# Kernel tuning notes

Hardware: AMD Instinct MI355X
Metric: run time of the kernel (lower is better)

## Reference

```python
import jax, jax.numpy as jnp
import numpy as np

B = 1_048_576
W = 64  # hidden width
N_FREQ = 6   # 3 dims * 6 freqs * (sin,cos) = 36
K_BLOB = 4   # one-blob bins per dim


def _freq_embed(p):
    # [B,3] -> [B,36]
    freqs = 2.0 ** jnp.arange(N_FREQ, dtype=p.dtype)
    ang = jnp.pi * p[:, :, None] * freqs  # [B,3,6]
    return jnp.concatenate([jnp.sin(ang), jnp.cos(ang)], axis=-1).reshape(p.shape[0], 3 * 2 * N_FREQ)


def _sph(d):
    # unit-square parameterization of a direction, [B,3] -> [B,2]
    d = d / (jnp.linalg.norm(d, axis=-1, keepdims=True) + 1e-8)
    u = jnp.arctan2(d[:, 1], d[:, 0]) / (2.0 * jnp.pi) + 0.5
    v = jnp.arccos(jnp.clip(d[:, 2], -1.0 + 1e-6, 1.0 - 1e-6)) / jnp.pi
    return jnp.stack([u, v], axis=-1)


def _one_blob(x, k=K_BLOB):
    # x in [0,1], [B,D] -> [B,D*k] Gaussian one-blob encoding
    centers = (jnp.arange(k, dtype=x.dtype) + 0.5) / k
    sigma = 1.0 / k
    g = jnp.exp(-0.5 * ((x[..., None] - centers) / sigma) ** 2)  # [B,D,k]
    return g.reshape(x.shape[0], -1)


def _encode(p, wi, n, alpha, beta, r):
    ones = jnp.ones((p.shape[0], 2), dtype=p.dtype)
    return jnp.concatenate([
        _freq_embed(p),                      # 36
        _one_blob(_sph(wi)),                 # 8
        _one_blob(_sph(n)),                  # 8
        _one_blob(1.0 - jnp.exp(-r)),        # 4
        alpha, beta,                         # 6
        ones,                                # 2 (implicit bias)
    ], axis=-1)                              # -> [B,64]


def _mlp(x, Ws):
    h = x
    for Wk in Ws[:-1]:
        h = jax.nn.relu(h @ Wk.T)
    return h @ Ws[-1].T  # [B,3]


def setup_inputs() -> dict:
    key = jax.random.key(0)
    ks = jax.random.split(key, 13)
    p = jax.random.normal(ks[0], (B, 3), jnp.float32)
    wi = jax.random.normal(ks[1], (B, 3), jnp.float32)
    n = jax.random.normal(ks[2], (B, 3), jnp.float32)
    alpha = jax.random.uniform(ks[3], (B, 3), jnp.float32)
    beta = jax.random.uniform(ks[4], (B, 3), jnp.float32)
    r = jax.random.uniform(ks[5], (B, 1), jnp.float32)
    s = 1.0 / np.sqrt(W)
    weights = {}
    for i in range(6):
        weights[f"W{i}"] = jax.random.normal(ks[6 + i], (W, W), jnp.float32) * s
    weights["W6"] = jax.random.normal(ks[12], (3, W), jnp.float32) * s
    return dict(p=p, wi=wi, n=n, alpha=alpha, beta=beta, r=r, **weights)


def reference(p, wi, n, alpha, beta, r, W0, W1, W2, W3, W4, W5, W6):
    x = _encode(p, wi, n, alpha, beta, r)
    out = _mlp(x, [W0, W1, W2, W3, W4, W5, W6])
    return out * (alpha + beta)  # reflectance factorization
```

## Files before the change

kernel.cpp:

```cpp
#include <hip/hip_runtime.h>


typedef _Float16 f16;
typedef f16 f16x2 __attribute__((ext_vector_type(2)));
typedef f16 f16x4 __attribute__((ext_vector_type(4)));
typedef f16 f16x8 __attribute__((ext_vector_type(8)));
typedef float f32x4 __attribute__((ext_vector_type(4)));

#define MFMA16(A, B, C) __builtin_amdgcn_mfma_f32_16x16x32_f16(A, B, C, 0, 0, 0)
#define LDS_FENCE() __asm__ volatile("" ::: "memory")

static constexpr int TILES = 4;
static constexpr int WAVES = 2;
static constexpr int BLOCK = WAVES * 64;
static constexpr int SPB   = WAVES * TILES * 16;

static constexpr int    WUNITS   = 50;
static constexpr size_t WS_BYTES = (size_t)WUNITS * 64 * 16;

__device__ __forceinline__ f16x2 pkh(float a, float b) {
    return __builtin_bit_cast(f16x2, __builtin_amdgcn_cvt_pkrtz(a, b));
}

__device__ __forceinline__ f16x8 pack8(const float* f) {
    f16x2 a = pkh(f[0], f[1]);
    f16x2 b = pkh(f[2], f[3]);
    f16x2 c = pkh(f[4], f[5]);
    f16x2 d = pkh(f[6], f[7]);
    f16x8 v;
    v[0] = a[0]; v[1] = a[1]; v[2] = b[0]; v[3] = b[1];
    v[4] = c[0]; v[5] = c[1]; v[6] = d[0]; v[7] = d[1];
    return v;
}

__device__ __forceinline__ f16x8 load_wfrag(const float* __restrict__ Wl, int row, int k0) {
    const f32x4 lo = *(const f32x4*)(Wl + row * 64 + k0);
    const f32x4 hi = *(const f32x4*)(Wl + row * 64 + k0 + 4);
    float t[8] = {lo[0], lo[1], lo[2], lo[3], hi[0], hi[1], hi[2], hi[3]};
    return pack8(t);
}

__device__ __forceinline__ float fast_atan2_rev(float y, float x) {
    const float ax = __builtin_fabsf(x), ay = __builtin_fabsf(y);
    const float mx = fmaxf(ax, ay), mn = fminf(ax, ay);
    const float a = mn * __builtin_amdgcn_rcpf(fmaxf(mx, 1e-30f));
    const float s = a * a;
    float r = a * (0.99997726f + s * (-0.33262347f + s * (0.19354346f +
              s * (-0.11643287f + s * (0.05265332f - s * 0.01172120f)))));
    if (ay > ax) r = 1.5707963268f - r;
    if (x < 0.0f) r = 3.1415926536f - r;
    r = (y < 0.0f) ? -r : r;
    return r * 0.15915494309189535f;
}

__device__ __forceinline__ float fast_acos(float x) {
    const float ax = __builtin_fabsf(x);
    const float t = __builtin_amdgcn_sqrtf(1.0f - ax);
    const float p = t * (1.5707288f + ax * (-0.2121144f +
                    ax * (0.0742610f - ax * 0.0187293f)));
    return (x < 0.0f) ? (3.1415926536f - p) : p;
}

__global__ __launch_bounds__(256, 1) void pack_weights_kernel(
    const float* __restrict__ W0, const float* __restrict__ W1,
    const float* __restrict__ W2, const float* __restrict__ W3,
    const float* __restrict__ W4, const float* __restrict__ W5,
    const float* __restrict__ W6, f16* __restrict__ ws)
{
    const int u = (int)blockIdx.x * 256 + threadIdx.x;
    if (u >= WUNITS * 64) return;
    const int lane = u & 63;
    const int unit = u >> 6;
    const int q = lane >> 4, m = lane & 15;
    f16x8 v;
    if (unit < 48) {
        const int l = unit >> 3, frag = unit & 7;
        const int kt = frag >> 2, mt = frag & 3;
        const float* Ws[6] = {W0, W1, W2, W3, W4, W5};
        const float* __restrict__ Wl = Ws[l];
        const int row = mt * 16 + m, col0 = kt * 32 + q * 8;
#pragma unroll
        for (int j = 0; j < 8; ++j) v[j] = (f16)Wl[row * 64 + col0 + j];
    } else {
        const int kt = unit - 48;
        const int col0 = kt * 32 + q * 8;
#pragma unroll
        for (int j = 0; j < 8; ++j)
            v[j] = (m < 3) ? (f16)W6[m * 64 + col0 + j] : (f16)0.0f;
    }
    *(f16x8*)(ws + unit * 512 + lane * 8) = v;
}

template<int PACKED>
__global__ __launch_bounds__(BLOCK, 3) void nrc_mlp_kernel(
    const float* __restrict__ P,  const float* __restrict__ WI,
    const float* __restrict__ NV, const float* __restrict__ AL,
    const float* __restrict__ BE, const float* __restrict__ RR,
    const f16*   __restrict__ ws,
    const float* __restrict__ W0, const float* __restrict__ W1,
    const float* __restrict__ W2, const float* __restrict__ W3,
    const float* __restrict__ W4, const float* __restrict__ W5,
    const float* __restrict__ W6, float* __restrict__ Out)
{
    __shared__ __attribute__((aligned(16)))
        unsigned char smem[WAVES * TILES * 2048 + WAVES * TILES * 16 * 16];

    const int tid  = threadIdx.x;
    const int lane = tid & 63;
    const int w    = tid >> 6;
    const int q    = lane >> 4;
    const int m    = lane & 15;

    unsigned char* const hb  = smem + w * (TILES * 2048);
    unsigned char* const abb = smem + WAVES * TILES * 2048 + w * (TILES * 16 * 16);

    const int wave_base = (int)blockIdx.x * SPB + w * (TILES * 16);

    {
        const int s = wave_base + lane;

        float pv[3], wv[3], nv[3], av[3], bv[3];
#pragma unroll
        for (int d = 0; d < 3; ++d) {
            pv[d] = P [s * 3 + d];
            wv[d] = WI[s * 3 + d];
            nv[d] = NV[s * 3 + d];
            av[d] = AL[s * 3 + d];
            bv[d] = BE[s * 3 + d];
        }
        const float rv = RR[s];

        float feat[64];
#pragma unroll
        for (int d = 0; d < 3; ++d) {
#pragma unroll
            for (int k = 0; k < 6; ++k) {
                const float rev = pv[d] * (0.5f * (float)(1 << k));
                const float fr  = __builtin_amdgcn_fractf(rev);
                feat[d * 12 + k]     = __builtin_amdgcn_sinf(fr);
                feat[d * 12 + 6 + k] = __builtin_amdgcn_cosf(fr);
            }
        }
#pragma unroll
        for (int which = 0; which < 2; ++which) {
            const float* dv = (which == 0) ? wv : nv;
            const int fo = 36 + which * 8;
            const float nr = __builtin_amdgcn_sqrtf(dv[0]*dv[0] + dv[1]*dv[1] + dv[2]*dv[2]) + 1e-8f;
            const float u  = fast_atan2_rev(dv[1], dv[0]) + 0.5f;
            float zc = dv[2] * __builtin_amdgcn_rcpf(nr);
            zc = fminf(fmaxf(zc, -1.0f + 1e-6f), 1.0f - 1e-6f);
            const float vv = fast_acos(zc) * 0.3183098861837907f;
#pragma unroll
            for (int i = 0; i < 4; ++i) {
                const float cc = (i + 0.5f) * 0.25f;
                const float du = u - cc, dvv = vv - cc;
                feat[fo + i]     = __expf(-8.0f * du * du);
                feat[fo + 4 + i] = __expf(-8.0f * dvv * dvv);
            }
        }
        {
            const float x = 1.0f - __expf(-rv);
#pragma unroll
            for (int i = 0; i < 4; ++i) {
                const float cc = (i + 0.5f) * 0.25f;
                const float dx = x - cc;
                feat[52 + i] = __expf(-8.0f * dx * dx);
            }
        }
        feat[56] = av[0]; feat[57] = av[1]; feat[58] = av[2];
        feat[59] = bv[0]; feat[60] = bv[1]; feat[61] = bv[2];
        feat[62] = 1.0f;  feat[63] = 1.0f;

        f32x4 abv;
        abv[0] = av[0] + bv[0]; abv[1] = av[1] + bv[1];
        abv[2] = av[2] + bv[2]; abv[3] = 0.0f;
        *(f32x4*)(abb + lane * 16) = abv;

        unsigned char* const tb = hb + q * 2048;
#pragma unroll
        for (int fc = 0; fc < 8; ++fc) {
            f16x8 v = pack8(&feat[fc * 8]);
            *(f16x8*)(tb + fc * 256 + m * 16) = v;
        }
    }
    LDS_FENCE();

    const f16* const wbase = ws + (size_t)lane * 8;
    const float* const Ws[6] = {W0, W1, W2, W3, W4, W5};

#pragma unroll
    for (int layer = 0; layer < 6; ++layer) {
        f16x8 wf[8];
        if (PACKED) {
#pragma unroll
            for (int f = 0; f < 8; ++f)
                wf[f] = *(const f16x8*)(wbase + (layer * 8 + f) * 512);
        } else {
            const float* __restrict__ Wl = Ws[layer];
#pragma unroll
            for (int kt = 0; kt < 2; ++kt)
#pragma unroll
                for (int mt = 0; mt < 4; ++mt)
                    wf[kt * 4 + mt] = load_wfrag(Wl, mt * 16 + m, kt * 32 + q * 8);
        }

        f16x8 bf[TILES][2];
#pragma unroll
        for (int t = 0; t < TILES; ++t) {
            unsigned char* const tb = hb + t * 2048;
            bf[t][0] = *(const f16x8*)(tb +        q * 256 + m * 16);
            bf[t][1] = *(const f16x8*)(tb + 1024 + q * 256 + m * 16);
        }
        LDS_FENCE();

#pragma unroll
        for (int t = 0; t < TILES; ++t) {
            unsigned char* const tb = hb + t * 2048;
            f32x4 acc[4];
#pragma unroll
            for (int mt = 0; mt < 4; ++mt) {
                f32x4 z = {0.0f, 0.0f, 0.0f, 0.0f};
                z = MFMA16(wf[mt],     bf[t][0], z);
                z = MFMA16(wf[4 + mt], bf[t][1], z);
                acc[mt] = z;
            }
#pragma unroll
            for (int mt = 0; mt < 4; ++mt) {
                const float r0 = fmaxf(acc[mt][0], 0.0f);
                const float r1 = fmaxf(acc[mt][1], 0.0f);
                const float r2 = fmaxf(acc[mt][2], 0.0f);
                const float r3 = fmaxf(acc[mt][3], 0.0f);
                const f16x2 lo = pkh(r0, r1);
                const f16x2 hi = pkh(r2, r3);
                f16x4 v;
                v[0] = lo[0]; v[1] = lo[1]; v[2] = hi[0]; v[3] = hi[1];
                *(f16x4*)(tb + (mt * 2 + (q >> 1)) * 256 + m * 16 + (q & 1) * 8) = v;
            }
        }
        LDS_FENCE();
    }

    {
        f16x8 w6f0, w6f1;
        if (PACKED) {
            w6f0 = *(const f16x8*)(wbase + 48 * 512);
            w6f1 = *(const f16x8*)(wbase + 49 * 512);
        } else {
            float t0[8], t1[8];
#pragma unroll
            for (int j = 0; j < 8; ++j) {
                t0[j] = (m < 3) ? W6[m * 64 +      q * 8 + j] : 0.0f;
                t1[j] = (m < 3) ? W6[m * 64 + 32 + q * 8 + j] : 0.0f;
            }
            w6f0 = pack8(t0);
            w6f1 = pack8(t1);
        }
#pragma unroll
        for (int t = 0; t < TILES; ++t) {
            unsigned char* const tb = hb + t * 2048;
            const f16x8 bf0 = *(const f16x8*)(tb +        q * 256 + m * 16);
            const f16x8 bf1 = *(const f16x8*)(tb + 1024 + q * 256 + m * 16);
            f32x4 z = {0.0f, 0.0f, 0.0f, 0.0f};
            z = MFMA16(w6f0, bf0, z);
            z = MFMA16(w6f1, bf1, z);
            const f32x4 abv = *(const f32x4*)(abb + (t * 16 + m) * 16);
            if (lane < 16) {
                const int s = wave_base + t * 16 + m;
                float* o = Out + s * 3;
                o[0] = z[0] * abv[0];
                o[1] = z[1] * abv[1];
                o[2] = z[2] * abv[2];
            }
        }
    }
}

extern "C" void kernel_launch(void* const* d_in, const int* in_sizes, int n_in,
                              void* d_out, int out_size, void* d_ws, size_t ws_size,
                              hipStream_t stream) {
    (void)n_in; (void)out_size;
    const float* P  = (const float*)d_in[0];
    const float* WI = (const float*)d_in[1];
    const float* NV = (const float*)d_in[2];
    const float* AL = (const float*)d_in[3];
    const float* BE = (const float*)d_in[4];
    const float* RR = (const float*)d_in[5];
    const float* W0 = (const float*)d_in[6];
    const float* W1 = (const float*)d_in[7];
    const float* W2 = (const float*)d_in[8];
    const float* W3 = (const float*)d_in[9];
    const float* W4 = (const float*)d_in[10];
    const float* W5 = (const float*)d_in[11];
    const float* W6 = (const float*)d_in[12];
    f16*   ws  = (f16*)d_ws;
    float* Out = (float*)d_out;

    const int Bn = in_sizes[0] / 3;
    const int grid = Bn / SPB;

    if (ws_size >= WS_BYTES) {
        hipLaunchKernelGGL(pack_weights_kernel, dim3((WUNITS * 64 + 255) / 256),
                           dim3(256), 0, stream, W0, W1, W2, W3, W4, W5, W6, ws);
        hipLaunchKernelGGL((nrc_mlp_kernel<1>), dim3(grid), dim3(BLOCK), 0, stream,
                           P, WI, NV, AL, BE, RR, ws,
                           W0, W1, W2, W3, W4, W5, W6, Out);
    } else {
        hipLaunchKernelGGL((nrc_mlp_kernel<0>), dim3(grid), dim3(BLOCK), 0, stream,
                           P, WI, NV, AL, BE, RR, ws,
                           W0, W1, W2, W3, W4, W5, W6, Out);
    }
}
```

Measured before the change: 171.1 us.

## Keep MLP activations in registers via 16x16x16 MFMA layout chaining

Switches from 16x16x32 to 16x16x16 f16 MFMA. The output fragment layout of each layer then matches the B-operand layout of the next, so hidden activations stay in registers across all six layers instead of going through LDS every layer. Weight packing is reordered to the new K-block layout, and blocks shrink to one wave with a higher occupancy hint. The risks are twice as many MFMA instructions at a lower per-instruction K, and extra register pressure from holding four tiles of activations.

```diff
diff --git a/kernel.cpp b/kernel.cpp
--- a/kernel.cpp
+++ b/kernel.cpp
@@ -7,13 +7,12 @@
 typedef f16 f16x8 __attribute__((ext_vector_type(8)));
 typedef float f32x4 __attribute__((ext_vector_type(4)));
 
-#define MFMA16(A, B, C) __builtin_amdgcn_mfma_f32_16x16x32_f16(A, B, C, 0, 0, 0)
+#define MFMA16(A, B, C) __builtin_amdgcn_mfma_f32_16x16x16f16(A, B, C, 0, 0, 0)
 #define LDS_FENCE() __asm__ volatile("" ::: "memory")
 
 static constexpr int TILES = 4;
-static constexpr int WAVES = 2;
-static constexpr int BLOCK = WAVES * 64;
-static constexpr int SPB   = WAVES * TILES * 16;
+static constexpr int BLOCK = 64;
+static constexpr int SPB   = 64;
 
 static constexpr int    WUNITS   = 50;
 static constexpr size_t WS_BYTES = (size_t)WUNITS * 64 * 16;
@@ -33,11 +32,12 @@
     return v;
 }
 
-__device__ __forceinline__ f16x8 load_wfrag(const float* __restrict__ Wl, int row, int k0) {
-    const f32x4 lo = *(const f32x4*)(Wl + row * 64 + k0);
-    const f32x4 hi = *(const f32x4*)(Wl + row * 64 + k0 + 4);
-    float t[8] = {lo[0], lo[1], lo[2], lo[3], hi[0], hi[1], hi[2], hi[3]};
-    return pack8(t);
+__device__ __forceinline__ f16x4 pack4(f32x4 v) {
+    f16x2 a = pkh(v[0], v[1]);
+    f16x2 b = pkh(v[2], v[3]);
+    f16x4 r;
+    r[0] = a[0]; r[1] = a[1]; r[2] = b[0]; r[3] = b[1];
+    return r;
 }
 
 __device__ __forceinline__ float fast_atan2_rev(float y, float x) {
@@ -74,25 +74,35 @@
     const int q = lane >> 4, m = lane & 15;
     f16x8 v;
     if (unit < 48) {
-        const int l = unit >> 3, frag = unit & 7;
-        const int kt = frag >> 2, mt = frag & 3;
+        const int l = unit >> 3, rem = unit & 7;
+        const int mt = rem >> 1, kbh = rem & 1;
         const float* Ws[6] = {W0, W1, W2, W3, W4, W5};
         const float* __restrict__ Wl = Ws[l];
-        const int row = mt * 16 + m, col0 = kt * 32 + q * 8;
-#pragma unroll
-        for (int j = 0; j < 8; ++j) v[j] = (f16)Wl[row * 64 + col0 + j];
+#pragma unroll
+        for (int e = 0; e < 8; ++e) {
+            const int kb = kbh * 2 + (e >> 2), j = e & 3;
+            v[e] = (f16)Wl[(mt * 16 + m) * 64 + kb * 16 + q * 4 + j];
+        }
     } else {
-        const int kt = unit - 48;
-        const int col0 = kt * 32 + q * 8;
-#pragma unroll
-        for (int j = 0; j < 8; ++j)
-            v[j] = (m < 3) ? (f16)W6[m * 64 + col0 + j] : (f16)0.0f;
+        const int kbh = unit - 48;
+#pragma unroll
+        for (int e = 0; e < 8; ++e) {
+            const int kb = kbh * 2 + (e >> 2), j = e & 3;
+            v[e] = (m < 3) ? (f16)W6[m * 64 + kb * 16 + q * 4 + j] : (f16)0.0f;
+        }
     }
     *(f16x8*)(ws + unit * 512 + lane * 8) = v;
 }
 
+__device__ __forceinline__ f16x4 lo4(f16x8 v) {
+    return __builtin_shufflevector(v, v, 0, 1, 2, 3);
+}
+__device__ __forceinline__ f16x4 hi4(f16x8 v) {
+    return __builtin_shufflevector(v, v, 4, 5, 6, 7);
+}
+
 template<int PACKED>
-__global__ __launch_bounds__(BLOCK, 3) void nrc_mlp_kernel(
+__global__ __launch_bounds__(BLOCK, 4) void nrc_mlp_kernel(
     const float* __restrict__ P,  const float* __restrict__ WI,
     const float* __restrict__ NV, const float* __restrict__ AL,
     const float* __restrict__ BE, const float* __restrict__ RR,
@@ -102,19 +112,15 @@
     const float* __restrict__ W4, const float* __restrict__ W5,
     const float* __restrict__ W6, float* __restrict__ Out)
 {
-    __shared__ __attribute__((aligned(16)))
-        unsigned char smem[WAVES * TILES * 2048 + WAVES * TILES * 16 * 16];
-
-    const int tid  = threadIdx.x;
-    const int lane = tid & 63;
-    const int w    = tid >> 6;
+    __shared__ __attribute__((aligned(16))) unsigned char smem[TILES * 2048 + TILES * 16 * 16];
+
+    const int lane = threadIdx.x & 63;
     const int q    = lane >> 4;
     const int m    = lane & 15;
-
-    unsigned char* const hb  = smem + w * (TILES * 2048);
-    unsigned char* const abb = smem + WAVES * TILES * 2048 + w * (TILES * 16 * 16);
-
-    const int wave_base = (int)blockIdx.x * SPB + w * (TILES * 16);
+    unsigned char* const hb  = smem;
+    unsigned char* const abb = smem + TILES * 2048;
+
+    const int wave_base = (int)blockIdx.x * SPB;
 
     {
         const int s = wave_base + lane;
@@ -176,93 +182,88 @@
         abv[2] = av[2] + bv[2]; abv[3] = 0.0f;
         *(f32x4*)(abb + lane * 16) = abv;
 
-        unsigned char* const tb = hb + q * 2048;
-#pragma unroll
-        for (int fc = 0; fc < 8; ++fc) {
-            f16x8 v = pack8(&feat[fc * 8]);
-            *(f16x8*)(tb + fc * 256 + m * 16) = v;
+        const int te = lane >> 4, me = lane & 15;
+        unsigned char* const tb = hb + te * 2048 + me * 128;
+#pragma unroll
+        for (int g = 0; g < 8; ++g) {
+            const int slot0 = (4 * g + 4 * me) & 31;
+            *(f16x8*)(tb + slot0 * 4) = pack8(&feat[g * 8]);
         }
     }
     LDS_FENCE();
+
+    f16x4 bf[TILES][4];
+#pragma unroll
+    for (int t = 0; t < TILES; ++t) {
+#pragma unroll
+        for (int kb = 0; kb < 4; ++kb) {
+            const int s0 = (kb * 8 + q * 2 + 4 * m) & 31;
+            bf[t][kb] = *(const f16x4*)(hb + t * 2048 + m * 128 + s0 * 4);
+        }
+    }
 
     const f16* const wbase = ws + (size_t)lane * 8;
     const float* const Ws[6] = {W0, W1, W2, W3, W4, W5};
+    const f16x4 zero4 = {(f16)0.0f, (f16)0.0f, (f16)0.0f, (f16)0.0f};
 
 #pragma unroll
     for (int layer = 0; layer < 6; ++layer) {
-        f16x8 wf[8];
+        f16x4 wa[4][4];
         if (PACKED) {
 #pragma unroll
-            for (int f = 0; f < 8; ++f)
-                wf[f] = *(const f16x8*)(wbase + (layer * 8 + f) * 512);
+            for (int i = 0; i < 8; ++i) {
+                const f16x8 v = *(const f16x8*)(wbase + (layer * 8 + i) * 512);
+                const int mt = i >> 1, kbh = i & 1;
+                wa[mt][kbh * 2]     = lo4(v);
+                wa[mt][kbh * 2 + 1] = hi4(v);
+            }
         } else {
             const float* __restrict__ Wl = Ws[layer];
 #pragma unroll
-            for (int kt = 0; kt < 2; ++kt)
-#pragma unroll
-                for (int mt = 0; mt < 4; ++mt)
-                    wf[kt * 4 + mt] = load_wfrag(Wl, mt * 16 + m, kt * 32 + q * 8);
-        }
-
-        f16x8 bf[TILES][2];
+            for (int mt = 0; mt < 4; ++mt)
+#pragma unroll
+                for (int kb = 0; kb < 4; ++kb)
+                    wa[mt][kb] = pack4(*(const f32x4*)(Wl + (mt * 16 + m) * 64 + kb * 16 + q * 4));
+        }
+
 #pragma unroll
         for (int t = 0; t < TILES; ++t) {
-            unsigned char* const tb = hb + t * 2048;
-            bf[t][0] = *(const f16x8*)(tb +        q * 256 + m * 16);
-            bf[t][1] = *(const f16x8*)(tb + 1024 + q * 256 + m * 16);
-        }
-        LDS_FENCE();
-
-#pragma unroll
-        for (int t = 0; t < TILES; ++t) {
-            unsigned char* const tb = hb + t * 2048;
             f32x4 acc[4];
 #pragma unroll
             for (int mt = 0; mt < 4; ++mt) {
                 f32x4 z = {0.0f, 0.0f, 0.0f, 0.0f};
-                z = MFMA16(wf[mt],     bf[t][0], z);
-                z = MFMA16(wf[4 + mt], bf[t][1], z);
+#pragma unroll
+                for (int kb = 0; kb < 4; ++kb)
+                    z = MFMA16(wa[mt][kb], bf[t][kb], z);
                 acc[mt] = z;
             }
 #pragma unroll
-            for (int mt = 0; mt < 4; ++mt) {
-                const float r0 = fmaxf(acc[mt][0], 0.0f);
-                const float r1 = fmaxf(acc[mt][1], 0.0f);
-                const float r2 = fmaxf(acc[mt][2], 0.0f);
-                const float r3 = fmaxf(acc[mt][3], 0.0f);
-                const f16x2 lo = pkh(r0, r1);
-                const f16x2 hi = pkh(r2, r3);
-                f16x4 v;
-                v[0] = lo[0]; v[1] = lo[1]; v[2] = hi[0]; v[3] = hi[1];
-                *(f16x4*)(tb + (mt * 2 + (q >> 1)) * 256 + m * 16 + (q & 1) * 8) = v;
-            }
-        }
-        LDS_FENCE();
+            for (int mt = 0; mt < 4; ++mt)
+                bf[t][mt] = __builtin_elementwise_max(pack4(acc[mt]), zero4);
+        }
     }
 
     {
-        f16x8 w6f0, w6f1;
+        f16x4 w6a[4];
         if (PACKED) {
-            w6f0 = *(const f16x8*)(wbase + 48 * 512);
-            w6f1 = *(const f16x8*)(wbase + 49 * 512);
+            const f16x8 v0 = *(const f16x8*)(wbase + 48 * 512);
+            const f16x8 v1 = *(const f16x8*)(wbase + 49 * 512);
+            w6a[0] = lo4(v0); w6a[1] = hi4(v0);
+            w6a[2] = lo4(v1); w6a[3] = hi4(v1);
         } else {
-            float t0[8], t1[8];
-#pragma unroll
-            for (int j = 0; j < 8; ++j) {
-                t0[j] = (m < 3) ? W6[m * 64 +      q * 8 + j] : 0.0f;
-                t1[j] = (m < 3) ? W6[m * 64 + 32 + q * 8 + j] : 0.0f;
-            }
-            w6f0 = pack8(t0);
-            w6f1 = pack8(t1);
+#pragma unroll
+            for (int kb = 0; kb < 4; ++kb) {
+                f32x4 t4 = {0.0f, 0.0f, 0.0f, 0.0f};
+                if (m < 3) t4 = *(const f32x4*)(W6 + m * 64 + kb * 16 + q * 4);
+                w6a[kb] = pack4(t4);
+            }
         }
 #pragma unroll
         for (int t = 0; t < TILES; ++t) {
-            unsigned char* const tb = hb + t * 2048;
-            const f16x8 bf0 = *(const f16x8*)(tb +        q * 256 + m * 16);
-            const f16x8 bf1 = *(const f16x8*)(tb + 1024 + q * 256 + m * 16);
             f32x4 z = {0.0f, 0.0f, 0.0f, 0.0f};
-            z = MFMA16(w6f0, bf0, z);
-            z = MFMA16(w6f1, bf1, z);
+#pragma unroll
+            for (int kb = 0; kb < 4; ++kb)
+                z = MFMA16(w6a[kb], bf[t][kb], z);
             const f32x4 abv = *(const f32x4*)(abb + (t * 16 + m) * 16);
             if (lane < 16) {
                 const int s = wave_base + t * 16 + m;
```

Measured after the change: 170.1 us. About the same (-0.6%).
